# Performance work log

Hardware: AMD Instinct MI355X
Metric: run time of the kernel (lower is better)

The kernel has to match this reference:

```python
import jax, jax.numpy as jnp
import numpy as np

TOPK = 2


def setup_inputs() -> dict:
    key = jax.random.key(0)
    k1, k2 = jax.random.split(key)
    B, N, D, E, C = 4, 2048, 2048, 8, 512
    token_inputs = jax.random.normal(k1, (B, N, D), dtype=jnp.float32)
    # bottleneck_in.weight.t() stacked over experts: [E, D, C]; scaled like a real init
    bottleneck_weights = jax.random.normal(k2, (E, D, C), dtype=jnp.float32) * 0.02
    return {
        "token_inputs": token_inputs,
        "bottleneck_weights": bottleneck_weights,
        "expert_capacity": 640,
    }


def _routing(router_probs, expert_capacity, topk):
    # router_probs: [B, N, E]
    B, N, E = router_probs.shape
    _, expert_indices = jax.lax.top_k(router_probs, topk)      # [B, N, topk]
    idx = jnp.transpose(expert_indices, (0, 2, 1)).reshape(B, topk * N)
    expert_mask = jax.nn.one_hot(idx, E, dtype=jnp.int32)       # [B, topk*N, E]
    token_priority = jnp.cumsum(expert_mask, axis=1) * expert_mask - 1
    token_priority = token_priority.reshape(B, topk, N, E)
    token_priority = jnp.transpose(token_priority, (0, 2, 1, 3))  # [B, N, topk, E]
    token_priority = jnp.max(token_priority, axis=2)              # [B, N, E]
    # one-hot over capacity; negative (-1) and >= capacity priorities map to all-zero rows
    cap_range = jnp.arange(expert_capacity, dtype=jnp.int32)
    dispatch = (token_priority[..., None] == cap_range).astype(jnp.float32)  # [B,N,E,C]
    combine = router_probs[..., None] * dispatch                            # [B,N,E,C]
    return dispatch, combine


def reference(token_inputs, bottleneck_weights, expert_capacity):
    # activation_cache: [B, N, E, Cb]
    activation_cache = jnp.einsum("bnd,edc->bnec", token_inputs, bottleneck_weights)
    router_logits = jnp.sqrt(jnp.sum(activation_cache * activation_cache, axis=-1))  # [B,N,E]
    router_probs = jax.nn.softmax(router_logits, axis=-1)
    dispatch, combine = _routing(router_probs, expert_capacity, TOPK)
    return jnp.stack([dispatch, combine], axis=0)  # [2, B, N, E, capacity]
```

## Files before the change

### kernel.cpp

```cpp
#include <hip/hip_runtime.h>
#include <math.h>

constexpr int Bb = 4, Nn = 2048, Dd = 2048, Ee = 8, Cbn = 512;
constexpr int Mm = Bb * Nn;

typedef _Float16 half8 __attribute__((ext_vector_type(8)));
typedef float floatx16 __attribute__((ext_vector_type(16)));

#define GLL16(g, l)                                                     \
  __builtin_amdgcn_global_load_lds(                                     \
      (const __attribute__((address_space(1))) void*)(g),               \
      (__attribute__((address_space(3))) void*)(l), 16, 0, 0)

__global__ __launch_bounds__(256) void transpose_w(const float* __restrict__ W,
                                                   _Float16* __restrict__ WThi,
                                                   _Float16* __restrict__ WTlo) {
  const int kt = blockIdx.x;
  const int ct = blockIdx.y;
  const int e = blockIdx.z;
  __shared__ _Float16 thi[64][72];
  __shared__ _Float16 tlo[64][72];
  const int tx = threadIdx.x & 15, ty = threadIdx.x >> 4;
  const float* src = W + ((size_t)(e * 2048 + kt * 64)) * 512 + ct * 64;
#pragma unroll
  for (int p = 0; p < 4; ++p) {
    int kk = ty + p * 16;
    float4 v = *(const float4*)(src + (size_t)kk * 512 + tx * 4);
    _Float16 h;
    h = (_Float16)v.x; thi[tx * 4 + 0][kk] = h; tlo[tx * 4 + 0][kk] = (_Float16)(v.x - (float)h);
    h = (_Float16)v.y; thi[tx * 4 + 1][kk] = h; tlo[tx * 4 + 1][kk] = (_Float16)(v.y - (float)h);
    h = (_Float16)v.z; thi[tx * 4 + 2][kk] = h; tlo[tx * 4 + 2][kk] = (_Float16)(v.z - (float)h);
    h = (_Float16)v.w; thi[tx * 4 + 3][kk] = h; tlo[tx * 4 + 3][kk] = (_Float16)(v.w - (float)h);
  }
  __syncthreads();
  const int rr = threadIdx.x >> 3;
  const int ch = threadIdx.x & 7;
  _Float16* dh = WThi + ((size_t)(e * 512 + ct * 64)) * 2048 + kt * 64;
  _Float16* dl = WTlo + ((size_t)(e * 512 + ct * 64)) * 2048 + kt * 64;
#pragma unroll
  for (int p = 0; p < 2; ++p) {
    int cc = rr + p * 32;
    *(half8*)(dh + (size_t)cc * 2048 + ch * 8) = *(const half8*)(&thi[cc][ch * 8]);
    *(half8*)(dl + (size_t)cc * 2048 + ch * 8) = *(const half8*)(&tlo[cc][ch * 8]);
  }
}

__global__ __launch_bounds__(256) void gemm_mfma(const float* __restrict__ X,
                                                 const _Float16* __restrict__ WThi,
                                                 const _Float16* __restrict__ WTlo,
                                                 float* __restrict__ partial) {
  const int bid = blockIdx.x;
  const int st = bid >> 8;
  const int stm = st & 3;
  const int stn = st >> 2;
  const int li = bid & 255;
  const int mtile = stm * 16 + (li >> 4);
  const int ntile = stn * 16 + (li & 15);

  const int tid = threadIdx.x;
  const int wave = tid >> 6, lane = tid & 63;
  const int wm = wave >> 1, wn = wave & 1;
  const int h = lane >> 5;

  __shared__ __align__(16) char lds[32768];
  char* ldsA = lds;
  char* ldsBhi = lds + 16384;
  char* ldsBlo = lds + 24576;

  const int lrA = lane >> 3;
  const int cposA = lane & 7;
  const int cgA = cposA ^ lrA;
  const float* xg[4];
  int ldsAoff[4];
#pragma unroll
  for (int q = 0; q < 4; ++q) {
    const int row = wave * 32 + q * 8 + lrA;
    xg[q] = X + (size_t)(mtile * 128 + row) * 2048 + cgA * 4;
    ldsAoff[q] = (wave * 32 + q * 8) * 128;
  }

  const int lrB = lane >> 2;
  const int cposB = lane & 3;
  const int cgB = cposB ^ ((lrB >> 1) & 3);
  const int rB0s = wave * 32 + lrB;
  const int rB1s = rB0s + 16;
  const _Float16* wh0 = WThi + (size_t)(ntile * 128 + rB0s) * 2048 + cgB * 8;
  const _Float16* wh1 = WThi + (size_t)(ntile * 128 + rB1s) * 2048 + cgB * 8;
  const _Float16* wl0 = WTlo + (size_t)(ntile * 128 + rB0s) * 2048 + cgB * 8;
  const _Float16* wl1 = WTlo + (size_t)(ntile * 128 + rB1s) * 2048 + cgB * 8;
  const int lqB0 = wave * 2048;
  const int lqB1 = lqB0 + 1024;

  const int keyA = lane & 7;
  const int rowA0 = wm * 64 + (lane & 31);
  const int rowA1 = rowA0 + 32;
  int oAf0[2][2], oAf1[2][2];
#pragma unroll
  for (int s = 0; s < 2; ++s)
#pragma unroll
    for (int c = 0; c < 2; ++c) {
      const int g = s * 4 + h * 2 + c;
      oAf0[s][c] = rowA0 * 128 + ((g ^ keyA) << 4);
      oAf1[s][c] = rowA1 * 128 + ((g ^ keyA) << 4);
    }

  const int rB0 = wn * 64 + (lane & 31);
  const int rB1 = rB0 + 32;
  auto foffB = [&](int r, int s) {
    return r * 64 + (((s * 2 + h) ^ ((r >> 1) & 3)) << 4);
  };
  const int oB0[2] = {foffB(rB0, 0), foffB(rB0, 1)};
  const int oB1[2] = {foffB(rB1, 0), foffB(rB1, 1)};

  floatx16 acc00 = {}, acc01 = {}, acc10 = {}, acc11 = {};

  auto cvtA = [](const char* p0, const char* p1, half8& ah, half8& al) {
    float4 f0 = *(const float4*)p0;
    float4 f1 = *(const float4*)p1;
    float xf[8] = {f0.x, f0.y, f0.z, f0.w, f1.x, f1.y, f1.z, f1.w};
#pragma unroll
    for (int j = 0; j < 8; ++j) {
      _Float16 hv = (_Float16)xf[j];
      ah[j] = hv;
      al[j] = (_Float16)(xf[j] - (float)hv);
    }
  };

  for (int kt = 0; kt < 64; ++kt) {
    const int k0 = kt * 32;
#pragma unroll
    for (int q = 0; q < 4; ++q) GLL16(xg[q] + k0, ldsA + ldsAoff[q]);
    GLL16(wh0 + k0, ldsBhi + lqB0);
    GLL16(wh1 + k0, ldsBhi + lqB1);
    GLL16(wl0 + k0, ldsBlo + lqB0);
    GLL16(wl1 + k0, ldsBlo + lqB1);
    __syncthreads();
#pragma unroll
    for (int s = 0; s < 2; ++s) {
      half8 ah0, al0, ah1, al1;
      cvtA(ldsA + oAf0[s][0], ldsA + oAf0[s][1], ah0, al0);
      cvtA(ldsA + oAf1[s][0], ldsA + oAf1[s][1], ah1, al1);
      half8 bh0 = *(const half8*)(ldsBhi + oB0[s]);
      half8 bh1 = *(const half8*)(ldsBhi + oB1[s]);
      half8 bl0 = *(const half8*)(ldsBlo + oB0[s]);
      half8 bl1 = *(const half8*)(ldsBlo + oB1[s]);
      acc00 = __builtin_amdgcn_mfma_f32_32x32x16_f16(ah0, bh0, acc00, 0, 0, 0);
      acc00 = __builtin_amdgcn_mfma_f32_32x32x16_f16(ah0, bl0, acc00, 0, 0, 0);
      acc00 = __builtin_amdgcn_mfma_f32_32x32x16_f16(al0, bh0, acc00, 0, 0, 0);
      acc01 = __builtin_amdgcn_mfma_f32_32x32x16_f16(ah0, bh1, acc01, 0, 0, 0);
      acc01 = __builtin_amdgcn_mfma_f32_32x32x16_f16(ah0, bl1, acc01, 0, 0, 0);
      acc01 = __builtin_amdgcn_mfma_f32_32x32x16_f16(al0, bh1, acc01, 0, 0, 0);
      acc10 = __builtin_amdgcn_mfma_f32_32x32x16_f16(ah1, bh0, acc10, 0, 0, 0);
      acc10 = __builtin_amdgcn_mfma_f32_32x32x16_f16(ah1, bl0, acc10, 0, 0, 0);
      acc10 = __builtin_amdgcn_mfma_f32_32x32x16_f16(al1, bh0, acc10, 0, 0, 0);
      acc11 = __builtin_amdgcn_mfma_f32_32x32x16_f16(ah1, bh1, acc11, 0, 0, 0);
      acc11 = __builtin_amdgcn_mfma_f32_32x32x16_f16(ah1, bl1, acc11, 0, 0, 0);
      acc11 = __builtin_amdgcn_mfma_f32_32x32x16_f16(al1, bh1, acc11, 0, 0, 0);
    }
    __syncthreads();
  }

  float myv = 0.f;
#pragma unroll
  for (int i = 0; i < 2; ++i) {
    const floatx16& c0 = i ? acc10 : acc00;
    const floatx16& c1 = i ? acc11 : acc01;
#pragma unroll
    for (int reg = 0; reg < 16; ++reg) {
      float v = c0[reg] * c0[reg] + c1[reg] * c1[reg];
#pragma unroll
      for (int m = 1; m <= 16; m <<= 1) v += __shfl_xor(v, m, 64);
      if ((lane & 31) == i * 16 + reg) myv = v;
    }
  }
  {
    const int i = (lane & 31) >> 4;
    const int reg = lane & 15;
    const int row = i * 32 + (reg & 3) + 8 * (reg >> 2) + 4 * h;
    const int token = mtile * 128 + wm * 64 + row;
    const int slice = ntile * 2 + wn;
    partial[(size_t)token * 64 + slice] = myv;
  }
}

__global__ void route_kernel(const float* __restrict__ partial,
                             int* __restrict__ idx1, int* __restrict__ idx2,
                             float* __restrict__ p1, float* __restrict__ p2) {
  int t = blockIdx.x * blockDim.x + threadIdx.x;
  if (t >= Mm) return;
  float l[Ee];
  float mx = -1e30f;
#pragma unroll
  for (int e = 0; e < Ee; ++e) {
    float s = 0.f;
#pragma unroll
    for (int u = 0; u < 8; ++u) s += partial[(size_t)t * 64 + e * 8 + u];
    l[e] = sqrtf(s);
    mx = fmaxf(mx, l[e]);
  }
  float p[Ee];
  float s = 0.f;
#pragma unroll
  for (int e = 0; e < Ee; ++e) {
    p[e] = expf(l[e] - mx);
    s += p[e];
  }
  float inv = 1.f / s;
  int i1 = 0;
  float b1 = l[0];
#pragma unroll
  for (int e = 1; e < Ee; ++e)
    if (l[e] > b1) { b1 = l[e]; i1 = e; }
  int i2 = -1;
  float b2 = -1e30f;
#pragma unroll
  for (int e = 0; e < Ee; ++e)
    if (e != i1 && l[e] > b2) { b2 = l[e]; i2 = e; }
  idx1[t] = i1;
  idx2[t] = i2;
  p1[t] = p[i1] * inv;
  p2[t] = p[i2] * inv;
}

__global__ void scan_kernel(const int* __restrict__ idx1,
                            const int* __restrict__ idx2,
                            int* __restrict__ prios) {
  const int b = blockIdx.x;
  const int tid = threadIdx.x;
  __shared__ int cnts[256][8];
  int cnt[8] = {0, 0, 0, 0, 0, 0, 0, 0};
  int eloc[16];
  const int base_p = tid * 16;
#pragma unroll
  for (int i = 0; i < 16; ++i) {
    int p = base_p + i;
    int k = p >> 11;
    int n = p & (Nn - 1);
    int e = (k == 0 ? idx1 : idx2)[b * Nn + n];
    eloc[i] = e;
    cnt[e]++;
  }
#pragma unroll
  for (int e = 0; e < 8; ++e) cnts[tid][e] = cnt[e];
  __syncthreads();
  if (tid < 8) {
    int run = 0;
    for (int i = 0; i < 256; ++i) {
      int v = cnts[i][tid];
      cnts[i][tid] = run;
      run += v;
    }
  }
  __syncthreads();
  int base[8];
#pragma unroll
  for (int e = 0; e < 8; ++e) base[e] = cnts[tid][e];
#pragma unroll
  for (int i = 0; i < 16; ++i) {
    int e = eloc[i];
    prios[b * 2 * Nn + base_p + i] = base[e]++;
  }
}

__global__ void zero_kernel(float4* __restrict__ out, int n4) {
  int i = blockIdx.x * blockDim.x + threadIdx.x;
  if (i < n4) out[i] = make_float4(0.f, 0.f, 0.f, 0.f);
}

__global__ void scatter_kernel(const int* __restrict__ idx1,
                               const int* __restrict__ idx2,
                               const float* __restrict__ p1,
                               const float* __restrict__ p2,
                               const int* __restrict__ prios,
                               float* __restrict__ out, int cap) {
  int t = blockIdx.x * blockDim.x + threadIdx.x;
  if (t >= Mm) return;
  int b = t >> 11;
  int n = t & (Nn - 1);
  size_t disp = (size_t)t * Ee * cap;
  size_t comb = disp + (size_t)Mm * Ee * cap;
  {
    int e = idx1[t];
    int p = prios[b * 2 * Nn + n];
    if (p < cap) {
      out[disp + (size_t)e * cap + p] = 1.f;
      out[comb + (size_t)e * cap + p] = p1[t];
    }
  }
  {
    int e = idx2[t];
    int p = prios[b * 2 * Nn + Nn + n];
    if (p < cap) {
      out[disp + (size_t)e * cap + p] = 1.f;
      out[comb + (size_t)e * cap + p] = p2[t];
    }
  }
}

extern "C" void kernel_launch(void* const* d_in, const int* in_sizes, int n_in,
                              void* d_out, int out_size, void* d_ws, size_t ws_size,
                              hipStream_t stream) {
  const float* X = (const float*)d_in[0];
  const float* W = (const float*)d_in[1];
  float* out = (float*)d_out;
  const int cap = out_size / (2 * Bb * Nn * Ee);

  char* ws = (char*)d_ws;
  _Float16* WThi = (_Float16*)ws;
  _Float16* WTlo = (_Float16*)(ws + 16777216ull);
  float* partial = (float*)(ws + 33554432ull);
  int* idx1 = (int*)(ws + 35651584ull);
  int* idx2 = idx1 + Mm;
  float* p1 = (float*)(idx2 + Mm);
  float* p2 = p1 + Mm;
  int* prios = (int*)(p2 + Mm);

  transpose_w<<<dim3(32, 8, 8), 256, 0, stream>>>(W, WThi, WTlo);
  gemm_mfma<<<2048, 256, 0, stream>>>(X, WThi, WTlo, partial);
  route_kernel<<<Mm / 256, 256, 0, stream>>>(partial, idx1, idx2, p1, p2);
  scan_kernel<<<Bb, 256, 0, stream>>>(idx1, idx2, prios);
  const int n4 = out_size / 4;
  zero_kernel<<<(n4 + 255) / 256, 256, 0, stream>>>((float4*)out, n4);
  scatter_kernel<<<Mm / 256, 256, 0, stream>>>(idx1, idx2, p1, p2, prios, out, cap);
}
```

Before: 854.8 us.

## Pre-split X to fp16 tiled layout, double-buffer GEMM LDS, fuse zero with scatter

```diff
diff --git a/kernel.cpp b/kernel.cpp
--- a/kernel.cpp
+++ b/kernel.cpp
@@ -12,9 +12,11 @@
       (const __attribute__((address_space(1))) void*)(g),               \
       (__attribute__((address_space(3))) void*)(l), 16, 0, 0)
 
+#define MFMA_F16(a, b, c) __builtin_amdgcn_mfma_f32_32x32x16_f16(a, b, c, 0, 0, 0)
+
+
 __global__ __launch_bounds__(256) void transpose_w(const float* __restrict__ W,
-                                                   _Float16* __restrict__ WThi,
-                                                   _Float16* __restrict__ WTlo) {
+                                                   _Float16* __restrict__ WT) {
   const int kt = blockIdx.x;
   const int ct = blockIdx.y;
   const int e = blockIdx.z;
@@ -26,28 +28,57 @@
   for (int p = 0; p < 4; ++p) {
     int kk = ty + p * 16;
     float4 v = *(const float4*)(src + (size_t)kk * 512 + tx * 4);
-    _Float16 h;
-    h = (_Float16)v.x; thi[tx * 4 + 0][kk] = h; tlo[tx * 4 + 0][kk] = (_Float16)(v.x - (float)h);
-    h = (_Float16)v.y; thi[tx * 4 + 1][kk] = h; tlo[tx * 4 + 1][kk] = (_Float16)(v.y - (float)h);
-    h = (_Float16)v.z; thi[tx * 4 + 2][kk] = h; tlo[tx * 4 + 2][kk] = (_Float16)(v.z - (float)h);
-    h = (_Float16)v.w; thi[tx * 4 + 3][kk] = h; tlo[tx * 4 + 3][kk] = (_Float16)(v.w - (float)h);
-  }
-  __syncthreads();
-  const int rr = threadIdx.x >> 3;
-  const int ch = threadIdx.x & 7;
-  _Float16* dh = WThi + ((size_t)(e * 512 + ct * 64)) * 2048 + kt * 64;
-  _Float16* dl = WTlo + ((size_t)(e * 512 + ct * 64)) * 2048 + kt * 64;
+    _Float16 hh;
+    hh = (_Float16)v.x; thi[tx * 4 + 0][kk] = hh; tlo[tx * 4 + 0][kk] = (_Float16)(v.x - (float)hh);
+    hh = (_Float16)v.y; thi[tx * 4 + 1][kk] = hh; tlo[tx * 4 + 1][kk] = (_Float16)(v.y - (float)hh);
+    hh = (_Float16)v.z; thi[tx * 4 + 2][kk] = hh; tlo[tx * 4 + 2][kk] = (_Float16)(v.z - (float)hh);
+    hh = (_Float16)v.w; thi[tx * 4 + 3][kk] = hh; tlo[tx * 4 + 3][kk] = (_Float16)(v.w - (float)hh);
+  }
+  __syncthreads();
+  const int ntile = e * 4 + (ct >> 1);
 #pragma unroll
   for (int p = 0; p < 2; ++p) {
-    int cc = rr + p * 32;
-    *(half8*)(dh + (size_t)cc * 2048 + ch * 8) = *(const half8*)(&thi[cc][ch * 8]);
-    *(half8*)(dl + (size_t)cc * 2048 + ch * 8) = *(const half8*)(&tlo[cc][ch * 8]);
-  }
-}
-
-__global__ __launch_bounds__(256) void gemm_mfma(const float* __restrict__ X,
-                                                 const _Float16* __restrict__ WThi,
-                                                 const _Float16* __restrict__ WTlo,
+    int unit = threadIdx.x + p * 256;
+    int ch = unit >> 6;
+    int cc = unit & 63;
+    int ktile = kt * 2 + (ch >> 2);
+    int chunk = ch & 3;
+    int row = (ct & 1) * 64 + cc;
+    _Float16* dst = WT + ((size_t)(ntile * 64 + ktile)) * 8192 + chunk * 1024 + row * 8;
+    *(half8*)dst = *(const half8*)(&thi[cc][ch * 8]);
+    *(half8*)(dst + 4096) = *(const half8*)(&tlo[cc][ch * 8]);
+  }
+}
+
+__global__ __launch_bounds__(256) void split_x(const float* __restrict__ X,
+                                               _Float16* __restrict__ XT) {
+  const int mt = blockIdx.x;
+  const int kt = blockIdx.y;
+  const int tid = threadIdx.x;
+  _Float16* tb = XT + ((size_t)(mt * 64 + kt)) * 8192;
+#pragma unroll
+  for (int p = 0; p < 2; ++p) {
+    const int u = tid + p * 256;
+    const int chunk = u & 3;
+    const int row = u >> 2;
+    const float* src = X + ((size_t)(mt * 128 + row)) * 2048 + kt * 32 + chunk * 8;
+    float4 a = *(const float4*)src;
+    float4 b = *(const float4*)(src + 4);
+    float f[8] = {a.x, a.y, a.z, a.w, b.x, b.y, b.z, b.w};
+    half8 hi, lo;
+#pragma unroll
+    for (int j = 0; j < 8; ++j) {
+      _Float16 hh = (_Float16)f[j];
+      hi[j] = hh;
+      lo[j] = (_Float16)(f[j] - (float)hh);
+    }
+    *(half8*)(tb + chunk * 1024 + row * 8) = hi;
+    *(half8*)(tb + 4096 + chunk * 1024 + row * 8) = lo;
+  }
+}
+
+__global__ __launch_bounds__(256) void gemm_mfma(const _Float16* __restrict__ XT,
+                                                 const _Float16* __restrict__ WT,
                                                  float* __restrict__ partial) {
   const int bid = blockIdx.x;
   const int st = bid >> 8;
@@ -62,100 +93,67 @@
   const int wm = wave >> 1, wn = wave & 1;
   const int h = lane >> 5;
 
-  __shared__ __align__(16) char lds[32768];
-  char* ldsA = lds;
-  char* ldsBhi = lds + 16384;
-  char* ldsBlo = lds + 24576;
-
-  const int lrA = lane >> 3;
-  const int cposA = lane & 7;
-  const int cgA = cposA ^ lrA;
-  const float* xg[4];
-  int ldsAoff[4];
+  __shared__ __align__(16) char lds[65536];
+
+  const char* aSrc = (const char*)XT + (size_t)mtile * 64 * 16384 + wave * 4096 + lane * 16;
+  const char* bSrc = (const char*)WT + (size_t)ntile * 64 * 16384 + wave * 4096 + lane * 16;
+
+  const int rowA0 = wm * 64 + (lane & 31);
+  const int rB0 = wn * 64 + (lane & 31);
+
+  int aOff[2][2], bOff[2][2];
+#pragma unroll
+  for (int s = 0; s < 2; ++s)
+#pragma unroll
+    for (int hl = 0; hl < 2; ++hl) {
+      aOff[s][hl] = hl * 8192 + (s * 2 + h) * 2048 + rowA0 * 16;
+      bOff[s][hl] = 16384 + hl * 8192 + (s * 2 + h) * 2048 + rB0 * 16;
+    }
+
+  floatx16 acc00 = {}, acc01 = {}, acc10 = {}, acc11 = {};
+
 #pragma unroll
   for (int q = 0; q < 4; ++q) {
-    const int row = wave * 32 + q * 8 + lrA;
-    xg[q] = X + (size_t)(mtile * 128 + row) * 2048 + cgA * 4;
-    ldsAoff[q] = (wave * 32 + q * 8) * 128;
-  }
-
-  const int lrB = lane >> 2;
-  const int cposB = lane & 3;
-  const int cgB = cposB ^ ((lrB >> 1) & 3);
-  const int rB0s = wave * 32 + lrB;
-  const int rB1s = rB0s + 16;
-  const _Float16* wh0 = WThi + (size_t)(ntile * 128 + rB0s) * 2048 + cgB * 8;
-  const _Float16* wh1 = WThi + (size_t)(ntile * 128 + rB1s) * 2048 + cgB * 8;
-  const _Float16* wl0 = WTlo + (size_t)(ntile * 128 + rB0s) * 2048 + cgB * 8;
-  const _Float16* wl1 = WTlo + (size_t)(ntile * 128 + rB1s) * 2048 + cgB * 8;
-  const int lqB0 = wave * 2048;
-  const int lqB1 = lqB0 + 1024;
-
-  const int keyA = lane & 7;
-  const int rowA0 = wm * 64 + (lane & 31);
-  const int rowA1 = rowA0 + 32;
-  int oAf0[2][2], oAf1[2][2];
-#pragma unroll
-  for (int s = 0; s < 2; ++s)
-#pragma unroll
-    for (int c = 0; c < 2; ++c) {
-      const int g = s * 4 + h * 2 + c;
-      oAf0[s][c] = rowA0 * 128 + ((g ^ keyA) << 4);
-      oAf1[s][c] = rowA1 * 128 + ((g ^ keyA) << 4);
-    }
-
-  const int rB0 = wn * 64 + (lane & 31);
-  const int rB1 = rB0 + 32;
-  auto foffB = [&](int r, int s) {
-    return r * 64 + (((s * 2 + h) ^ ((r >> 1) & 3)) << 4);
-  };
-  const int oB0[2] = {foffB(rB0, 0), foffB(rB0, 1)};
-  const int oB1[2] = {foffB(rB1, 0), foffB(rB1, 1)};
-
-  floatx16 acc00 = {}, acc01 = {}, acc10 = {}, acc11 = {};
-
-  auto cvtA = [](const char* p0, const char* p1, half8& ah, half8& al) {
-    float4 f0 = *(const float4*)p0;
-    float4 f1 = *(const float4*)p1;
-    float xf[8] = {f0.x, f0.y, f0.z, f0.w, f1.x, f1.y, f1.z, f1.w};
-#pragma unroll
-    for (int j = 0; j < 8; ++j) {
-      _Float16 hv = (_Float16)xf[j];
-      ah[j] = hv;
-      al[j] = (_Float16)(xf[j] - (float)hv);
-    }
-  };
+    GLL16(aSrc + q * 1024, lds + wave * 4096 + q * 1024);
+    GLL16(bSrc + q * 1024, lds + 16384 + wave * 4096 + q * 1024);
+  }
+  __syncthreads();
 
   for (int kt = 0; kt < 64; ++kt) {
-    const int k0 = kt * 32;
-#pragma unroll
-    for (int q = 0; q < 4; ++q) GLL16(xg[q] + k0, ldsA + ldsAoff[q]);
-    GLL16(wh0 + k0, ldsBhi + lqB0);
-    GLL16(wh1 + k0, ldsBhi + lqB1);
-    GLL16(wl0 + k0, ldsBlo + lqB0);
-    GLL16(wl1 + k0, ldsBlo + lqB1);
-    __syncthreads();
+    const int cur = kt & 1;
+    if (kt < 63) {
+      const char* a = aSrc + (size_t)(kt + 1) * 16384;
+      const char* b = bSrc + (size_t)(kt + 1) * 16384;
+      char* base = lds + (cur ^ 1) * 32768 + wave * 4096;
+#pragma unroll
+      for (int q = 0; q < 4; ++q) {
+        GLL16(a + q * 1024, base + q * 1024);
+        GLL16(b + q * 1024, base + 16384 + q * 1024);
+      }
+    }
+    const char* L = lds + cur * 32768;
 #pragma unroll
     for (int s = 0; s < 2; ++s) {
-      half8 ah0, al0, ah1, al1;
-      cvtA(ldsA + oAf0[s][0], ldsA + oAf0[s][1], ah0, al0);
-      cvtA(ldsA + oAf1[s][0], ldsA + oAf1[s][1], ah1, al1);
-      half8 bh0 = *(const half8*)(ldsBhi + oB0[s]);
-      half8 bh1 = *(const half8*)(ldsBhi + oB1[s]);
-      half8 bl0 = *(const half8*)(ldsBlo + oB0[s]);
-      half8 bl1 = *(const half8*)(ldsBlo + oB1[s]);
-      acc00 = __builtin_amdgcn_mfma_f32_32x32x16_f16(ah0, bh0, acc00, 0, 0, 0);
-      acc00 = __builtin_amdgcn_mfma_f32_32x32x16_f16(ah0, bl0, acc00, 0, 0, 0);
-      acc00 = __builtin_amdgcn_mfma_f32_32x32x16_f16(al0, bh0, acc00, 0, 0, 0);
-      acc01 = __builtin_amdgcn_mfma_f32_32x32x16_f16(ah0, bh1, acc01, 0, 0, 0);
-      acc01 = __builtin_amdgcn_mfma_f32_32x32x16_f16(ah0, bl1, acc01, 0, 0, 0);
-      acc01 = __builtin_amdgcn_mfma_f32_32x32x16_f16(al0, bh1, acc01, 0, 0, 0);
-      acc10 = __builtin_amdgcn_mfma_f32_32x32x16_f16(ah1, bh0, acc10, 0, 0, 0);
-      acc10 = __builtin_amdgcn_mfma_f32_32x32x16_f16(ah1, bl0, acc10, 0, 0, 0);
-      acc10 = __builtin_amdgcn_mfma_f32_32x32x16_f16(al1, bh0, acc10, 0, 0, 0);
-      acc11 = __builtin_amdgcn_mfma_f32_32x32x16_f16(ah1, bh1, acc11, 0, 0, 0);
-      acc11 = __builtin_amdgcn_mfma_f32_32x32x16_f16(ah1, bl1, acc11, 0, 0, 0);
-      acc11 = __builtin_amdgcn_mfma_f32_32x32x16_f16(al1, bh1, acc11, 0, 0, 0);
+      half8 ah0 = *(const half8*)(L + aOff[s][0]);
+      half8 ah1 = *(const half8*)(L + aOff[s][0] + 512);
+      half8 al0 = *(const half8*)(L + aOff[s][1]);
+      half8 al1 = *(const half8*)(L + aOff[s][1] + 512);
+      half8 bh0 = *(const half8*)(L + bOff[s][0]);
+      half8 bh1 = *(const half8*)(L + bOff[s][0] + 512);
+      half8 bl0 = *(const half8*)(L + bOff[s][1]);
+      half8 bl1 = *(const half8*)(L + bOff[s][1] + 512);
+      acc00 = MFMA_F16(ah0, bh0, acc00);
+      acc00 = MFMA_F16(ah0, bl0, acc00);
+      acc00 = MFMA_F16(al0, bh0, acc00);
+      acc01 = MFMA_F16(ah0, bh1, acc01);
+      acc01 = MFMA_F16(ah0, bl1, acc01);
+      acc01 = MFMA_F16(al0, bh1, acc01);
+      acc10 = MFMA_F16(ah1, bh0, acc10);
+      acc10 = MFMA_F16(ah1, bl0, acc10);
+      acc10 = MFMA_F16(al1, bh0, acc10);
+      acc11 = MFMA_F16(ah1, bh1, acc11);
+      acc11 = MFMA_F16(ah1, bl1, acc11);
+      acc11 = MFMA_F16(al1, bh1, acc11);
     }
     __syncthreads();
   }
@@ -262,37 +260,37 @@
   }
 }
 
-__global__ void zero_kernel(float4* __restrict__ out, int n4) {
-  int i = blockIdx.x * blockDim.x + threadIdx.x;
-  if (i < n4) out[i] = make_float4(0.f, 0.f, 0.f, 0.f);
-}
-
-__global__ void scatter_kernel(const int* __restrict__ idx1,
-                               const int* __restrict__ idx2,
-                               const float* __restrict__ p1,
-                               const float* __restrict__ p2,
-                               const int* __restrict__ prios,
-                               float* __restrict__ out, int cap) {
-  int t = blockIdx.x * blockDim.x + threadIdx.x;
-  if (t >= Mm) return;
-  int b = t >> 11;
-  int n = t & (Nn - 1);
-  size_t disp = (size_t)t * Ee * cap;
-  size_t comb = disp + (size_t)Mm * Ee * cap;
-  {
+__global__ __launch_bounds__(256) void zscatter_kernel(const int* __restrict__ idx1,
+                                                       const int* __restrict__ idx2,
+                                                       const float* __restrict__ p1,
+                                                       const float* __restrict__ p2,
+                                                       const int* __restrict__ prios,
+                                                       float* __restrict__ out, int cap) {
+  const int t = blockIdx.x;
+  const int ec = Ee * cap;
+  float4* o1 = (float4*)(out + (size_t)t * ec);
+  float4* o2 = (float4*)(out + (size_t)(Mm + t) * ec);
+  const float4 z = make_float4(0.f, 0.f, 0.f, 0.f);
+  const int n4 = ec / 4;
+  for (int i = threadIdx.x; i < n4; i += 256) {
+    o1[i] = z;
+    o2[i] = z;
+  }
+  __syncthreads();
+  if (threadIdx.x == 0) {
+    const int b = t >> 11;
+    const int n = t & (Nn - 1);
     int e = idx1[t];
     int p = prios[b * 2 * Nn + n];
     if (p < cap) {
-      out[disp + (size_t)e * cap + p] = 1.f;
-      out[comb + (size_t)e * cap + p] = p1[t];
-    }
-  }
-  {
-    int e = idx2[t];
-    int p = prios[b * 2 * Nn + Nn + n];
+      out[(size_t)t * ec + e * cap + p] = 1.f;
+      out[(size_t)(Mm + t) * ec + e * cap + p] = p1[t];
+    }
+    e = idx2[t];
+    p = prios[b * 2 * Nn + Nn + n];
     if (p < cap) {
-      out[disp + (size_t)e * cap + p] = 1.f;
-      out[comb + (size_t)e * cap + p] = p2[t];
+      out[(size_t)t * ec + e * cap + p] = 1.f;
+      out[(size_t)(Mm + t) * ec + e * cap + p] = p2[t];
     }
   }
 }
@@ -306,8 +304,7 @@
   const int cap = out_size / (2 * Bb * Nn * Ee);
 
   char* ws = (char*)d_ws;
-  _Float16* WThi = (_Float16*)ws;
-  _Float16* WTlo = (_Float16*)(ws + 16777216ull);
+  _Float16* WT = (_Float16*)ws;
   float* partial = (float*)(ws + 33554432ull);
   int* idx1 = (int*)(ws + 35651584ull);
   int* idx2 = idx1 + Mm;
@@ -315,11 +312,12 @@
   float* p2 = p1 + Mm;
   int* prios = (int*)(p2 + Mm);
 
-  transpose_w<<<dim3(32, 8, 8), 256, 0, stream>>>(W, WThi, WTlo);
-  gemm_mfma<<<2048, 256, 0, stream>>>(X, WThi, WTlo, partial);
+  _Float16* XT = (_Float16*)d_out;
+
+  transpose_w<<<dim3(32, 8, 8), 256, 0, stream>>>(W, WT);
+  split_x<<<dim3(64, 64), 256, 0, stream>>>(X, XT);
+  gemm_mfma<<<2048, 256, 0, stream>>>(XT, WT, partial);
   route_kernel<<<Mm / 256, 256, 0, stream>>>(partial, idx1, idx2, p1, p2);
   scan_kernel<<<Bb, 256, 0, stream>>>(idx1, idx2, prios);
-  const int n4 = out_size / 4;
-  zero_kernel<<<(n4 + 255) / 256, 256, 0, stream>>>((float4*)out, n4);
-  scatter_kernel<<<Mm / 256, 256, 0, stream>>>(idx1, idx2, p1, p2, prios, out, cap);
-}
+  zscatter_kernel<<<Mm, 256, 0, stream>>>(idx1, idx2, p1, p2, prios, out, cap);
+}
```

New measurement: 777.3 us. 1.1x faster.
